# Optimization experiments

Hardware: AMD Instinct MI355X
Metric: run time of the kernel (lower is better)

The kernel has to match this reference:

```python
import jax, jax.numpy as jnp
import numpy as np


def setup_inputs() -> dict:
    key = jax.random.key(0)
    k1, k2, k3 = jax.random.split(key, 3)
    B, F, K = 16384, 512, 1000
    D = jax.random.normal(k1, (B, F), dtype=jnp.float32)
    weight = jax.random.normal(k2, (K, F), dtype=jnp.float32)  # (out_features, in_features)
    gamma = jax.random.uniform(k3, (K,), dtype=jnp.float32)
    return {"D": D, "weight": weight, "gamma": gamma}


def reference(D, weight, gamma):
    # Squared Euclidean distance from each row of D to each centroid (row of weight),
    # computed via ||a||^2 + ||b||^2 - 2 a.b (mathematically equal to the broadcast
    # subtract-square-sum in the original torch forward with d_view=None).
    d_sq = jnp.sum(D * D, axis=1, keepdims=True)            # (B, 1)
    w_sq = jnp.sum(weight * weight, axis=1)                  # (K,)
    cross = jnp.einsum('bf,kf->bk', D, weight)               # (B, K)
    dist_sq = d_sq + w_sq[None, :] - 2.0 * cross             # (B, K)
    return -dist_sq * gamma                                  # (B, K)
```

## Files before the change

### kernel.cpp

```cpp
#include <hip/hip_runtime.h>
#include <hip/hip_bf16.h>
#include <stdint.h>

#define B_ROWS 16384
#define F_DIM  512
#define K_OUT  1000
#define K_PAD  1024

#define BM 256
#define BN 256
#define BK 64

typedef __attribute__((ext_vector_type(4))) float f32x4;
typedef __attribute__((ext_vector_type(8))) short short8;
typedef unsigned short u16;
typedef unsigned int   u32;

#define OFF_DB   0
#define OFF_WB   16777216
#define OFF_DSQ  (16777216 + 1048576)
#define OFF_WSQ  (16777216 + 1048576 + 65536)

__device__ __forceinline__ u16 f2bf(float f) {
  union { float f; u32 u; } v; v.f = f;
  u32 u = v.u;
  u32 r = (u + 0x7fffu + ((u >> 16) & 1u)) >> 16;
  return (u16)r;
}

__global__ void prep_D(const float* __restrict__ D, u16* __restrict__ Db,
                       float* __restrict__ dsq) {
  int w    = threadIdx.x >> 6;
  int lane = threadIdx.x & 63;
  int row  = blockIdx.x * 4 + w;
  const float* src = D + (size_t)row * F_DIM + lane * 8;
  float4 v0 = *(const float4*)src;
  float4 v1 = *(const float4*)(src + 4);
  float s = v0.x*v0.x + v0.y*v0.y + v0.z*v0.z + v0.w*v0.w
          + v1.x*v1.x + v1.y*v1.y + v1.z*v1.z + v1.w*v1.w;
#pragma unroll
  for (int off = 32; off >= 1; off >>= 1) s += __shfl_xor(s, off);
  if (lane == 0) dsq[row] = s;
  uint4 p;
  p.x = (u32)f2bf(v0.x) | ((u32)f2bf(v0.y) << 16);
  p.y = (u32)f2bf(v0.z) | ((u32)f2bf(v0.w) << 16);
  p.z = (u32)f2bf(v1.x) | ((u32)f2bf(v1.y) << 16);
  p.w = (u32)f2bf(v1.z) | ((u32)f2bf(v1.w) << 16);
  *(uint4*)(Db + (size_t)row * F_DIM + lane * 8) = p;
}

__global__ void prep_W(const float* __restrict__ W, u16* __restrict__ Wb,
                       float* __restrict__ wsq) {
  int w    = threadIdx.x >> 6;
  int lane = threadIdx.x & 63;
  int row  = blockIdx.x * 4 + w;
  uint4 p; p.x = p.y = p.z = p.w = 0u;
  float s = 0.f;
  if (row < K_OUT) {
    const float* src = W + (size_t)row * F_DIM + lane * 8;
    float4 v0 = *(const float4*)src;
    float4 v1 = *(const float4*)(src + 4);
    s = v0.x*v0.x + v0.y*v0.y + v0.z*v0.z + v0.w*v0.w
      + v1.x*v1.x + v1.y*v1.y + v1.z*v1.z + v1.w*v1.w;
    p.x = (u32)f2bf(v0.x) | ((u32)f2bf(v0.y) << 16);
    p.y = (u32)f2bf(v0.z) | ((u32)f2bf(v0.w) << 16);
    p.z = (u32)f2bf(v1.x) | ((u32)f2bf(v1.y) << 16);
    p.w = (u32)f2bf(v1.z) | ((u32)f2bf(v1.w) << 16);
  }
#pragma unroll
  for (int off = 32; off >= 1; off >>= 1) s += __shfl_xor(s, off);
  if (lane == 0) wsq[row] = s;
  *(uint4*)(Wb + (size_t)row * F_DIM + lane * 8) = p;
}

__device__ __forceinline__ void gload_lds16(const void* g, void* l) {
  __builtin_amdgcn_global_load_lds(
      (const __attribute__((address_space(1))) void*)g,
      (__attribute__((address_space(3))) void*)l,
      16, 0, 0);
}


#define READ_A(QM)                                                             \
  _Pragma("unroll") for (int mi2 = 0; mi2 < 4; ++mi2)                          \
  _Pragma("unroll") for (int kk = 0; kk < 2; ++kk) {                           \
    int r = wm * 128 + ((QM) * 4 + mi2) * 16 + lr;                             \
    a[mi2][kk] = *(const short8*)(sAc + r * 128 +                              \
                                  ((((kk << 2) + lk4) ^ (r & 7)) << 4));       \
  }

#define READ_B(QN)                                                             \
  _Pragma("unroll") for (int ni2 = 0; ni2 < 2; ++ni2)                          \
  _Pragma("unroll") for (int kk = 0; kk < 2; ++kk) {                           \
    int r = wn * 64 + ((QN) * 2 + ni2) * 16 + lr;                              \
    b[ni2][kk] = *(const short8*)(sBc + r * 128 +                              \
                                  ((((kk << 2) + lk4) ^ (r & 7)) << 4));       \
  }

#define STAGE(Q)                                                               \
  if (t < 7) {                                                                 \
    int r  = (Q) * 64 + srow;                                                  \
    int sc = s8 ^ (r & 7);                                                     \
    gload_lds16(Ag + (size_t)r * F_DIM + kbn + sc * 8,                         \
                sAn + (Q) * 8192 + w * 1024);                                  \
    gload_lds16(Bg + (size_t)r * F_DIM + kbn + sc * 8,                         \
                sBn + (Q) * 8192 + w * 1024);                                  \
  }

#define MFMA16(QM, QN)                                                         \
  __builtin_amdgcn_s_barrier();                                                \
  asm volatile("s_waitcnt lgkmcnt(0)" ::: "memory");                           \
  __builtin_amdgcn_sched_barrier(0);                                           \
  __builtin_amdgcn_s_setprio(1);                                               \
  _Pragma("unroll") for (int mi2 = 0; mi2 < 4; ++mi2)                          \
  _Pragma("unroll") for (int ni2 = 0; ni2 < 2; ++ni2)                          \
  _Pragma("unroll") for (int kk = 0; kk < 2; ++kk)                             \
    acc[(QM)*4 + mi2][(QN)*2 + ni2] =                                          \
        __builtin_amdgcn_mfma_f32_16x16x32_bf16(                               \
            a[mi2][kk], b[ni2][kk], acc[(QM)*4 + mi2][(QN)*2 + ni2], 0, 0, 0); \
  __builtin_amdgcn_s_setprio(0);                                               \
  __builtin_amdgcn_s_barrier();

__global__ __launch_bounds__(512, 2) void gemm_eps(
    const u16* __restrict__ A,
    const u16* __restrict__ Bw,
    const float* __restrict__ dsq,
    const float* __restrict__ wsq,
    const float* __restrict__ gamma,
    float* __restrict__ out) {
  __shared__ __align__(16) char lds[131072];

  const int tid  = threadIdx.x;
  const int w    = tid >> 6;
  const int lane = tid & 63;
  const int lr   = lane & 15;
  const int lk4  = lane >> 4;
  const int wm   = w >> 2;
  const int wn   = w & 3;

  const int bid = blockIdx.x;
  const int wg  = (bid & 7) * 32 + (bid >> 3);
  const int mt  = wg >> 2;
  const int nt  = wg & 3;
  const int m0  = mt * BM;
  const int n0  = nt * BN;

  const u16* Ag = A  + (size_t)m0 * F_DIM;
  const u16* Bg = Bw + (size_t)n0 * F_DIM;

  const int srow = w * 8 + (lane >> 3);
  const int s8   = lane & 7;

  f32x4 acc[8][4];
#pragma unroll
  for (int i = 0; i < 8; ++i)
#pragma unroll
    for (int j = 0; j < 4; ++j) acc[i][j] = (f32x4){0.f, 0.f, 0.f, 0.f};

#pragma unroll
  for (int q = 0; q < 4; ++q) {
    int r  = q * 64 + srow;
    int sc = s8 ^ (r & 7);
    gload_lds16(Ag + (size_t)r * F_DIM + sc * 8, lds + q * 8192 + w * 1024);
    gload_lds16(Bg + (size_t)r * F_DIM + sc * 8, lds + 32768 + q * 8192 + w * 1024);
  }
  __syncthreads();

#pragma unroll 2
  for (int t = 0; t < 8; ++t) {
    char* sAc = lds + (t & 1) * 65536;
    char* sBc = sAc + 32768;
    char* sAn = lds + ((t + 1) & 1) * 65536;
    char* sBn = sAn + 32768;
    const int kbn = (t + 1) * 64;
    short8 a[4][2], b[2][2];

    READ_A(0) READ_B(0) STAGE(0) MFMA16(0, 0)
    READ_B(1)           STAGE(1) MFMA16(0, 1)
    READ_A(1)           STAGE(2) MFMA16(1, 1)
    READ_B(0)           STAGE(3) MFMA16(1, 0)

    __syncthreads();
  }

  float g_[4], wq_[4];
#pragma unroll
  for (int ni = 0; ni < 4; ++ni) {
    int col = n0 + wn * 64 + ni * 16 + lr;
    g_[ni]  = (col < K_OUT) ? gamma[col] : 0.f;
    wq_[ni] = (col < K_OUT) ? wsq[col]   : 0.f;
  }
  float* ch = (float*)lds;
  const int rl = tid >> 3;
  const int cb = (tid & 7) << 2;
#pragma unroll
  for (int c = 0; c < 4; ++c) {
    __syncthreads();
    if (wm == (c >> 1)) {
#pragma unroll
      for (int mi2 = 0; mi2 < 4; ++mi2) {
        const int mi    = ((c & 1) << 2) + mi2;
        const int row_l = mi2 * 16 + lk4 * 4;
        const int grow  = m0 + c * 64 + row_l;
#pragma unroll
        for (int j = 0; j < 4; ++j) {
          float dq = dsq[grow + j];
#pragma unroll
          for (int ni = 0; ni < 4; ++ni) {
            ch[(row_l + j) * 260 + wn * 64 + ni * 16 + lr] =
                g_[ni] * (2.f * acc[mi][ni][j] - dq - wq_[ni]);
          }
        }
      }
    }
    __syncthreads();
#pragma unroll
    for (int s = 0; s < 8; ++s) {
      int col = cb + s * 32;
      if (n0 + col < K_OUT) {
        float4 v = *(const float4*)&ch[rl * 260 + col];
        *(float4*)&out[(size_t)(m0 + c * 64 + rl) * K_OUT + n0 + col] = v;
      }
    }
  }
}

extern "C" void kernel_launch(void* const* d_in, const int* in_sizes, int n_in,
                              void* d_out, int out_size, void* d_ws, size_t ws_size,
                              hipStream_t stream) {
  const float* D     = (const float*)d_in[0];
  const float* W     = (const float*)d_in[1];
  const float* gamma = (const float*)d_in[2];
  float* out = (float*)d_out;
  char*  ws  = (char*)d_ws;

  u16*   Db  = (u16*)(ws + OFF_DB);
  u16*   Wb  = (u16*)(ws + OFF_WB);
  float* dsq = (float*)(ws + OFF_DSQ);
  float* wsq = (float*)(ws + OFF_WSQ);

  prep_D<<<B_ROWS / 4, 256, 0, stream>>>(D, Db, dsq);
  prep_W<<<K_PAD / 4, 256, 0, stream>>>(W, Wb, wsq);

  gemm_eps<<<(B_ROWS / BM) * (K_PAD / BN), 512, 0, stream>>>(
      Db, Wb, dsq, wsq, gamma, out);
}
```

Measured before the change: 44.01 us.

## Merge prep kernels and restage GEMM prefetch with fine-grained vmcnt waits

Fuses the D and W bf16-conversion prep kernels into a single launch to remove one kernel launch. Reworks the GEMM main loop so that global-to-LDS prefetch is issued in A/B quarter chunks. Each chunk is gated by s_waitcnt vmcnt(6) plus a barrier rather than a full __syncthreads per iteration, so loads overlap MFMA phases more continuously. Prefetch now also runs on the last iteration, wrapping around to k=0 and wasting one tile load. The barrier/wait ordering is delicate and risks races if the counts are off.

```diff
diff --git a/kernel.cpp b/kernel.cpp
--- a/kernel.cpp
+++ b/kernel.cpp
@@ -28,49 +28,47 @@
   return (u16)r;
 }
 
-__global__ void prep_D(const float* __restrict__ D, u16* __restrict__ Db,
-                       float* __restrict__ dsq) {
+__global__ void prep(const float* __restrict__ D, const float* __restrict__ W,
+                     u16* __restrict__ Db, u16* __restrict__ Wb,
+                     float* __restrict__ dsq, float* __restrict__ wsq) {
   int w    = threadIdx.x >> 6;
   int lane = threadIdx.x & 63;
-  int row  = blockIdx.x * 4 + w;
-  const float* src = D + (size_t)row * F_DIM + lane * 8;
-  float4 v0 = *(const float4*)src;
-  float4 v1 = *(const float4*)(src + 4);
-  float s = v0.x*v0.x + v0.y*v0.y + v0.z*v0.z + v0.w*v0.w
-          + v1.x*v1.x + v1.y*v1.y + v1.z*v1.z + v1.w*v1.w;
-#pragma unroll
-  for (int off = 32; off >= 1; off >>= 1) s += __shfl_xor(s, off);
-  if (lane == 0) dsq[row] = s;
-  uint4 p;
-  p.x = (u32)f2bf(v0.x) | ((u32)f2bf(v0.y) << 16);
-  p.y = (u32)f2bf(v0.z) | ((u32)f2bf(v0.w) << 16);
-  p.z = (u32)f2bf(v1.x) | ((u32)f2bf(v1.y) << 16);
-  p.w = (u32)f2bf(v1.z) | ((u32)f2bf(v1.w) << 16);
-  *(uint4*)(Db + (size_t)row * F_DIM + lane * 8) = p;
-}
-
-__global__ void prep_W(const float* __restrict__ W, u16* __restrict__ Wb,
-                       float* __restrict__ wsq) {
-  int w    = threadIdx.x >> 6;
-  int lane = threadIdx.x & 63;
-  int row  = blockIdx.x * 4 + w;
-  uint4 p; p.x = p.y = p.z = p.w = 0u;
-  float s = 0.f;
-  if (row < K_OUT) {
-    const float* src = W + (size_t)row * F_DIM + lane * 8;
+  if (blockIdx.x < B_ROWS / 4) {
+    int row = blockIdx.x * 4 + w;
+    const float* src = D + (size_t)row * F_DIM + lane * 8;
     float4 v0 = *(const float4*)src;
     float4 v1 = *(const float4*)(src + 4);
-    s = v0.x*v0.x + v0.y*v0.y + v0.z*v0.z + v0.w*v0.w
-      + v1.x*v1.x + v1.y*v1.y + v1.z*v1.z + v1.w*v1.w;
+    float s = v0.x*v0.x + v0.y*v0.y + v0.z*v0.z + v0.w*v0.w
+            + v1.x*v1.x + v1.y*v1.y + v1.z*v1.z + v1.w*v1.w;
+#pragma unroll
+    for (int off = 32; off >= 1; off >>= 1) s += __shfl_xor(s, off);
+    if (lane == 0) dsq[row] = s;
+    uint4 p;
     p.x = (u32)f2bf(v0.x) | ((u32)f2bf(v0.y) << 16);
     p.y = (u32)f2bf(v0.z) | ((u32)f2bf(v0.w) << 16);
     p.z = (u32)f2bf(v1.x) | ((u32)f2bf(v1.y) << 16);
     p.w = (u32)f2bf(v1.z) | ((u32)f2bf(v1.w) << 16);
-  }
-#pragma unroll
-  for (int off = 32; off >= 1; off >>= 1) s += __shfl_xor(s, off);
-  if (lane == 0) wsq[row] = s;
-  *(uint4*)(Wb + (size_t)row * F_DIM + lane * 8) = p;
+    *(uint4*)(Db + (size_t)row * F_DIM + lane * 8) = p;
+  } else {
+    int row = (blockIdx.x - B_ROWS / 4) * 4 + w;
+    uint4 p; p.x = p.y = p.z = p.w = 0u;
+    float s = 0.f;
+    if (row < K_OUT) {
+      const float* src = W + (size_t)row * F_DIM + lane * 8;
+      float4 v0 = *(const float4*)src;
+      float4 v1 = *(const float4*)(src + 4);
+      s = v0.x*v0.x + v0.y*v0.y + v0.z*v0.z + v0.w*v0.w
+        + v1.x*v1.x + v1.y*v1.y + v1.z*v1.z + v1.w*v1.w;
+      p.x = (u32)f2bf(v0.x) | ((u32)f2bf(v0.y) << 16);
+      p.y = (u32)f2bf(v0.z) | ((u32)f2bf(v0.w) << 16);
+      p.z = (u32)f2bf(v1.x) | ((u32)f2bf(v1.y) << 16);
+      p.w = (u32)f2bf(v1.z) | ((u32)f2bf(v1.w) << 16);
+    }
+#pragma unroll
+    for (int off = 32; off >= 1; off >>= 1) s += __shfl_xor(s, off);
+    if (lane == 0) wsq[row] = s;
+    *(uint4*)(Wb + (size_t)row * F_DIM + lane * 8) = p;
+  }
 }
 
 __device__ __forceinline__ void gload_lds16(const void* g, void* l) {
@@ -97,18 +95,24 @@
                                   ((((kk << 2) + lk4) ^ (r & 7)) << 4));       \
   }
 
-#define STAGE(Q)                                                               \
-  if (t < 7) {                                                                 \
-    int r  = (Q) * 64 + srow;                                                  \
+#define STAGE_A(h)                                                             \
+  _Pragma("unroll") for (int j = 0; j < 2; ++j) {                              \
+    int r  = (h) * 64 + j * 128 + srow;                                        \
     int sc = s8 ^ (r & 7);                                                     \
     gload_lds16(Ag + (size_t)r * F_DIM + kbn + sc * 8,                         \
-                sAn + (Q) * 8192 + w * 1024);                                  \
-    gload_lds16(Bg + (size_t)r * F_DIM + kbn + sc * 8,                         \
-                sBn + (Q) * 8192 + w * 1024);                                  \
-  }
-
-#define MFMA16(QM, QN)                                                         \
-  __builtin_amdgcn_s_barrier();                                                \
+                sAn + (h) * 8192 + j * 16384 + w * 1024);                      \
+  }
+
+#define STAGE_B(q)                                                             \
+  _Pragma("unroll") for (int j = 0; j < 2; ++j) {                              \
+    int g  = j * 8 + w;                                                        \
+    int rb = ((g >> 2) << 6) + (q) * 32 + ((g & 3) << 3);                      \
+    int r  = rb + (lane >> 3);                                                 \
+    int sc = s8 ^ (r & 7);                                                     \
+    gload_lds16(Bg + (size_t)r * F_DIM + kbn + sc * 8, sBn + rb * 128);        \
+  }
+
+#define MFMA_Q(QM, QN)                                                         \
   asm volatile("s_waitcnt lgkmcnt(0)" ::: "memory");                           \
   __builtin_amdgcn_sched_barrier(0);                                           \
   __builtin_amdgcn_s_setprio(1);                                               \
@@ -121,6 +125,9 @@
   __builtin_amdgcn_s_setprio(0);                                               \
   __builtin_amdgcn_s_barrier();
 
+#define VM6  asm volatile("s_waitcnt vmcnt(6)" ::: "memory")
+#define BAR  __builtin_amdgcn_s_barrier()
+
 __global__ __launch_bounds__(512, 2) void gemm_eps(
     const u16* __restrict__ A,
     const u16* __restrict__ Bw,
@@ -157,14 +164,12 @@
 #pragma unroll
     for (int j = 0; j < 4; ++j) acc[i][j] = (f32x4){0.f, 0.f, 0.f, 0.f};
 
-#pragma unroll
-  for (int q = 0; q < 4; ++q) {
-    int r  = q * 64 + srow;
-    int sc = s8 ^ (r & 7);
-    gload_lds16(Ag + (size_t)r * F_DIM + sc * 8, lds + q * 8192 + w * 1024);
-    gload_lds16(Bg + (size_t)r * F_DIM + sc * 8, lds + 32768 + q * 8192 + w * 1024);
-  }
-  __syncthreads();
+  {
+    char* sAn = lds;
+    char* sBn = lds + 32768;
+    const int kbn = 0;
+    STAGE_A(0) STAGE_B(0) STAGE_B(1) STAGE_A(1)
+  }
 
 #pragma unroll 2
   for (int t = 0; t < 8; ++t) {
@@ -172,15 +177,21 @@
     char* sBc = sAc + 32768;
     char* sAn = lds + ((t + 1) & 1) * 65536;
     char* sBn = sAn + 32768;
-    const int kbn = (t + 1) * 64;
+    const int kbn = ((t + 1) & 7) * BK;
     short8 a[4][2], b[2][2];
 
-    READ_A(0) READ_B(0) STAGE(0) MFMA16(0, 0)
-    READ_B(1)           STAGE(1) MFMA16(0, 1)
-    READ_A(1)           STAGE(2) MFMA16(1, 1)
-    READ_B(0)           STAGE(3) MFMA16(1, 0)
-
-    __syncthreads();
+    STAGE_A(0) VM6; BAR;
+    READ_A(0) READ_B(0)
+    MFMA_Q(0, 0)
+    STAGE_B(0) VM6; BAR;
+    READ_B(1)
+    MFMA_Q(0, 1)
+    STAGE_B(1) VM6; BAR;
+    READ_A(1)
+    MFMA_Q(1, 1)
+    STAGE_A(1) BAR;
+    READ_B(0)
+    MFMA_Q(1, 0)
   }
 
   float g_[4], wq_[4];
@@ -239,8 +250,7 @@
   float* dsq = (float*)(ws + OFF_DSQ);
   float* wsq = (float*)(ws + OFF_WSQ);
 
-  prep_D<<<B_ROWS / 4, 256, 0, stream>>>(D, Db, dsq);
-  prep_W<<<K_PAD / 4, 256, 0, stream>>>(W, Wb, wsq);
+  prep<<<B_ROWS / 4 + K_PAD / 4, 256, 0, stream>>>(D, W, Db, Wb, dsq, wsq);
 
   gemm_eps<<<(B_ROWS / BM) * (K_PAD / BN), 512, 0, stream>>>(
       Db, Wb, dsq, wsq, gamma, out);
```

New measurement: 42.21 us. -4.1%, faster.
